# Kernel optimization log

Measured on AMD Instinct MI355X. Metric: run time of the kernel, lower is better.

## Reference

```python
import jax, jax.numpy as jnp
import numpy as np

NUM_HEADS = 16
HEAD_SIZE = 64
CTXT_LEN = 2048
N_EMBED = 1024
BATCH = 2


def setup_inputs() -> dict:
    key = jax.random.key(0)
    ks = jax.random.split(key, 5)
    s = 0.02  # realistic init scale for weights
    return {
        "x": jax.random.normal(ks[0], (BATCH, CTXT_LEN, N_EMBED), dtype=jnp.float32),
        "Wk": jax.random.normal(ks[1], (N_EMBED, NUM_HEADS * HEAD_SIZE), dtype=jnp.float32) * s,
        "bk": jnp.zeros((NUM_HEADS * HEAD_SIZE,), dtype=jnp.float32),
        "Wq": jax.random.normal(ks[2], (N_EMBED, NUM_HEADS * HEAD_SIZE), dtype=jnp.float32) * s,
        "bq": jnp.zeros((NUM_HEADS * HEAD_SIZE,), dtype=jnp.float32),
        "Wv": jax.random.normal(ks[3], (N_EMBED, NUM_HEADS * HEAD_SIZE), dtype=jnp.float32) * s,
        "bv": jnp.zeros((NUM_HEADS * HEAD_SIZE,), dtype=jnp.float32),
        "Wo": jax.random.normal(ks[4], (NUM_HEADS * HEAD_SIZE, N_EMBED), dtype=jnp.float32) * s,
        "bo": jnp.zeros((N_EMBED,), dtype=jnp.float32),
    }


def reference(x, Wk, bk, Wq, bq, Wv, bv, Wo, bo):
    B, T, E = x.shape
    H, D = NUM_HEADS, HEAD_SIZE
    # QKV projections -> [B, T, H, D]
    k = (x @ Wk + bk).reshape(B, T, H, D)
    q = (x @ Wq + bq).reshape(B, T, H, D)
    v = (x @ Wv + bv).reshape(B, T, H, D)
    # NOTE: source scales by 1/sqrt(n_embed), not 1/sqrt(head_size)
    scale = 1.0 / (E ** 0.5)
    wei = jnp.einsum('bthd,bshd->bhts', q, k) * scale  # [B, H, T, T]
    causal = jnp.tril(jnp.ones((T, T), dtype=bool))
    wei = jnp.where(causal, wei, -jnp.inf)
    wei = jax.nn.softmax(wei, axis=-1)
    # dropout p=0.0 -> identity
    out = jnp.einsum('bhts,bshd->bthd', wei, v).reshape(B, T, H * D)
    return out @ Wo + bo
```

## Files before the change

kernel.cpp:

```cpp
#include <hip/hip_runtime.h>

#define NH 16
#define HS 64
#define T_CTX 2048
#define NE 1024
#define NB 2
#define BT (NB*T_CTX)
#define HD (NH*HS)

typedef unsigned short u16;
typedef __bf16 bf16_t;
typedef bf16_t bf16x8 __attribute__((ext_vector_type(8)));
typedef float f32x4 __attribute__((ext_vector_type(4)));
typedef u16 u16x8 __attribute__((ext_vector_type(8)));
typedef u16 u16x4 __attribute__((ext_vector_type(4)));

#define GLDS(gp, lp) __builtin_amdgcn_global_load_lds( \
    (const __attribute__((address_space(1))) void*)(gp), \
    (__attribute__((address_space(3))) void*)(lp), 16, 0, 0)

__device__ __forceinline__ u16 f2bf(float f) {
  union { float f; unsigned u; } x; x.f = f;
  return (u16)((x.u + 0x7fffu + ((x.u >> 16) & 1u)) >> 16);
}
__device__ __forceinline__ float bf2f(u16 u) {
  union { unsigned u; float f; } x; x.u = ((unsigned)u) << 16;
  return x.f;
}
__device__ __forceinline__ unsigned pack_bf2(float hi, float lo) {
  union { float f; unsigned u; } H, L; H.f = hi; L.f = lo;
  return __builtin_amdgcn_perm(H.u + 0x8000u, L.u + 0x8000u, 0x07060302);
}

__global__ __launch_bounds__(256) void k_prep_x(const float* __restrict__ x,
                                                u16* __restrict__ xb) {
  int i = blockIdx.x * blockDim.x + threadIdx.x;
  float4 v = ((const float4*)x)[i];
  ushort4 o;
  o.x = f2bf(v.x); o.y = f2bf(v.y); o.z = f2bf(v.z); o.w = f2bf(v.w);
  ((ushort4*)xb)[i] = o;
}

__global__ __launch_bounds__(256) void k_prep_w(
    const float* __restrict__ W0, const float* __restrict__ W1,
    const float* __restrict__ W2, const float* __restrict__ W3,
    u16* __restrict__ T0, u16* __restrict__ T1,
    u16* __restrict__ T2, u16* __restrict__ T3) {
  const float* W; u16* T;
  switch (blockIdx.z) {
    case 0: W = W0; T = T0; break;
    case 1: W = W1; T = T1; break;
    case 2: W = W2; T = T2; break;
    default: W = W3; T = T3; break;
  }
  __shared__ u16 tile[64 * 72];
  int k0 = blockIdx.x * 64, n0 = blockIdx.y * 64;
  int tid = threadIdx.x;
#pragma unroll
  for (int it = 0; it < 4; ++it) {
    int ci = tid + it * 256;
    int k = ci >> 4, c = ci & 15;
    float4 v = *(const float4*)&W[(size_t)(k0 + k) * NE + n0 + c * 4];
    int n = c * 4;
    tile[(n + 0) * 72 + k] = f2bf(v.x);
    tile[(n + 1) * 72 + k] = f2bf(v.y);
    tile[(n + 2) * 72 + k] = f2bf(v.z);
    tile[(n + 3) * 72 + k] = f2bf(v.w);
  }
  __syncthreads();
#pragma unroll
  for (int it = 0; it < 2; ++it) {
    int co = tid + it * 256;
    int n = co >> 3, c = co & 7;
    u16x8 v = *(const u16x8*)&tile[n * 72 + c * 8];
    *(u16x8*)&T[(size_t)(n0 + n) * NE + k0 + c * 8] = v;
  }
}

__global__ __launch_bounds__(256) void k_gemm_qkv(
    const u16* __restrict__ xb, const u16* __restrict__ Wt,
    const float* __restrict__ bq, const float* __restrict__ bk,
    const float* __restrict__ bv, u16* __restrict__ Qw,
    u16* __restrict__ Kw, u16* __restrict__ Vtw) {
  __shared__ u16 sh[3 * 8192];
  const int z = blockIdx.z;
  const u16* W = Wt + (size_t)z * NE * HD;
  const float* bias = (z == 0) ? bq : (z == 1 ? bk : bv);
  const float scale = (z == 0) ? 0.03125f * 1.4426950408889634f : 1.0f;
  const int bx = blockIdx.x;
  const int xcd = bx & 7, ii = bx >> 3;
  const int m0 = (xcd + 8 * (ii & 3)) * 128;
  const int n0 = (ii >> 2) * 128;
  const int tid = threadIdx.x;
  const int lane = tid & 63, w = tid >> 6;
  const int wm = (w >> 1) * 64, wn = (w & 1) * 64, q = lane >> 4, l16 = lane & 15;
  const int qsw = q ^ ((l16 >> 1) & 3);

  auto stage = [&](int k0, int b) {
    u16* As = sh + b * 8192;
    u16* Bs = As + 4096;
#pragma unroll
    for (int s2 = 0; s2 < 2; ++s2) {
      int ci = w * 64 + lane + s2 * 256;
      int row = ci >> 2, cc = ci & 3;
      int cs = cc ^ ((row >> 1) & 3);
      GLDS(xb + (size_t)(m0 + row) * NE + k0 + cs * 8, As + (size_t)ci * 8);
      GLDS(W  + (size_t)(n0 + row) * NE + k0 + cs * 8, Bs + (size_t)ci * 8);
    }
  };

  f32x4 acc[4][4];
#pragma unroll
  for (int i = 0; i < 4; ++i)
#pragma unroll
    for (int j = 0; j < 4; ++j)
#pragma unroll
      for (int r = 0; r < 4; ++r) acc[i][j][r] = 0.f;

  stage(0, 0);
  stage(32, 1);
  for (int kt = 0; kt < 32; ++kt) {
    u16* As = sh + (kt % 3) * 8192;
    u16* Bs = As + 4096;
    if (kt + 1 < 32)
      asm volatile("s_waitcnt vmcnt(4)\n\ts_barrier" ::: "memory");
    else
      asm volatile("s_waitcnt vmcnt(0)\n\ts_barrier" ::: "memory");
    if (kt + 2 < 32) stage((kt + 2) * 32, (kt + 2) % 3);
    bf16x8 av[4], bv4[4];
#pragma unroll
    for (int i = 0; i < 4; ++i) av[i]  = *(const bf16x8*)&As[(wm + i * 16 + l16) * 32 + qsw * 8];
#pragma unroll
    for (int j = 0; j < 4; ++j) bv4[j] = *(const bf16x8*)&Bs[(wn + j * 16 + l16) * 32 + qsw * 8];
#pragma unroll
    for (int i = 0; i < 4; ++i)
#pragma unroll
      for (int j = 0; j < 4; ++j)
        acc[i][j] = __builtin_amdgcn_mfma_f32_16x16x32_bf16(av[i], bv4[j], acc[i][j], 0, 0, 0);
  }
  __syncthreads();
  u16* Es = sh;

  const int bb = m0 >> 11;
  if (z == 2) {
#pragma unroll
    for (int j = 0; j < 4; ++j) {
      int n = wn + j * 16 + l16;
      float bn = bias[n0 + n];
#pragma unroll
      for (int i = 0; i < 4; ++i) {
        int m = wm + i * 16 + q * 4;
        u16x4 pk;
#pragma unroll
        for (int r = 0; r < 4; ++r) pk[r] = f2bf(acc[i][j][r] + bn);
        *(u16x4*)&Es[n * 132 + m] = pk;
      }
    }
    __syncthreads();
#pragma unroll
    for (int it = 0; it < 8; ++it) {
      int idx = it * 256 + tid;
      int dl = idx >> 4, c = idx & 15;
      u16x8 v = *(const u16x8*)&Es[dl * 132 + c * 8];
      int ng = n0 + dl, h = ng >> 6, d = ng & 63;
      int tt = (m0 & (T_CTX - 1)) + c * 8;
      *(u16x8*)&Vtw[((size_t)((bb * NH + h) * HS + d)) * T_CTX + tt] = v;
    }
  } else {
    u16* dst = (z == 0) ? Qw : Kw;
#pragma unroll
    for (int j = 0; j < 4; ++j) {
      int n = wn + j * 16 + l16;
      float bn = bias[n0 + n];
#pragma unroll
      for (int i = 0; i < 4; ++i)
#pragma unroll
        for (int r = 0; r < 4; ++r) {
          int m = wm + i * 16 + q * 4 + r;
          Es[m * 132 + n] = f2bf((acc[i][j][r] + bn) * scale);
        }
    }
    __syncthreads();
#pragma unroll
    for (int it = 0; it < 8; ++it) {
      int idx = it * 256 + tid;
      int tl = idx >> 4, c = idx & 15;
      u16x8 v = *(const u16x8*)&Es[tl * 132 + c * 8];
      int ng = n0 + c * 8, h = ng >> 6, d = ng & 63;
      int tt = (m0 & (T_CTX - 1)) + tl;
      *(u16x8*)&dst[(((size_t)(bb * NH + h)) * T_CTX + tt) * HS + d] = v;
    }
  }
}

__device__ __forceinline__ void stage_kv(const u16* __restrict__ Kp,
                                         const u16* __restrict__ Vp,
                                         int k0, u16* KsB, u16* VsB, int tid) {
#pragma unroll
  for (int it = 0; it < 2; ++it) {
    int ci = tid + it * 256;
    int row = ci >> 3, cc = ci & 7;
    int prow = (row & 32) | ((row & 12) << 1) | ((row & 16) >> 2) | (row & 3);
    int sw = (cc ^ (row & 7)) * 8;
    GLDS(Kp + (size_t)(k0 + prow) * HS + sw, KsB + ci * 8);
    GLDS(Vp + (size_t)row * T_CTX + k0 + sw, VsB + ci * 8);
  }
}

__global__ __launch_bounds__(256) void k_attn(
    const u16* __restrict__ Qw, const u16* __restrict__ Kw,
    const u16* __restrict__ Vtw, u16* __restrict__ op0,
    u16* __restrict__ op1, u16* __restrict__ op2,
    float* __restrict__ lsum) {
  __shared__ u16 Ks[3 * 64 * 64];
  __shared__ u16 Vs[3 * 64 * 64];

  const int b = blockIdx.x;
  const int xcd = b & 7, ii = b >> 3;
  const int bh = xcd + 8 * (ii & 3);
  const int x = ii >> 2;
  const int qt = 15 - x / 3;
  const int part = x - (15 - qt) * 3;
  const int ntiles = 2 * (qt + 1);
  const int npt = (ntiles + 2) / 3;
  const int klo = part * npt;
  const int khi = min(klo + npt, ntiles);
  const int qbase = qt * 128;

  const u16* Qp = Qw + (size_t)bh * T_CTX * HS;
  const u16* Kp = Kw + (size_t)bh * T_CTX * HS;
  const u16* Vp = Vtw + (size_t)bh * HS * T_CTX;

  const int tid = threadIdx.x, lane = tid & 63, w = tid >> 6;
  const int q = lane >> 4, c = lane & 15;
  const int rbase = w * 32;

  bf16x8 aq[2][2];
#pragma unroll
  for (int i = 0; i < 2; ++i)
#pragma unroll
    for (int s = 0; s < 2; ++s)
      aq[i][s] = *(const bf16x8*)&Qp[(size_t)(qbase + rbase + i * 16 + c) * HS + s * 32 + q * 8];

  f32x4 o[2][4];
  float lrow[2] = {0.f, 0.f};
#pragma unroll
  for (int i = 0; i < 2; ++i)
#pragma unroll
    for (int j = 0; j < 4; ++j)
#pragma unroll
      for (int r = 0; r < 4; ++r) o[i][j][r] = 0.f;

  if (klo < khi)     stage_kv(Kp, Vp, klo * 64,       Ks,        Vs,        tid);
  if (klo + 1 < khi) stage_kv(Kp, Vp, (klo + 1) * 64, Ks + 4096, Vs + 4096, tid);

  for (int kt = klo; kt < khi; ++kt) {
    const int k0 = kt * 64;
    const int idx = kt - klo;
    u16* KsB = Ks + (idx % 3) * 4096;
    u16* VsB = Vs + (idx % 3) * 4096;
    if (kt + 1 < khi) {
      asm volatile("s_waitcnt vmcnt(4)\n\ts_barrier" ::: "memory");
    } else {
      asm volatile("s_waitcnt vmcnt(0)\n\ts_barrier" ::: "memory");
    }
    if (kt + 2 < khi)
      stage_kv(Kp, Vp, (kt + 2) * 64,
               Ks + ((idx + 2) % 3) * 4096, Vs + ((idx + 2) % 3) * 4096, tid);

    f32x4 s[4][2];
#pragma unroll
    for (int i2 = 0; i2 < 4; ++i2) {
      int krow = i2 * 16 + c;
      bf16x8 kf0 = *(const bf16x8*)&KsB[krow * 64 + ((0 + q) ^ (krow & 7)) * 8];
      bf16x8 kf1 = *(const bf16x8*)&KsB[krow * 64 + ((4 + q) ^ (krow & 7)) * 8];
#pragma unroll
      for (int j2 = 0; j2 < 2; ++j2) {
        f32x4 z4 = {0.f, 0.f, 0.f, 0.f};
        z4 = __builtin_amdgcn_mfma_f32_16x16x32_bf16(kf0, aq[j2][0], z4, 0, 0, 0);
        s[i2][j2] = __builtin_amdgcn_mfma_f32_16x16x32_bf16(kf1, aq[j2][1], z4, 0, 0, 0);
      }
    }

    if (k0 + 63 > qbase + rbase) {
#pragma unroll
      for (int i2 = 0; i2 < 4; ++i2)
#pragma unroll
        for (int j2 = 0; j2 < 2; ++j2)
#pragma unroll
          for (int r = 0; r < 4; ++r) {
            int key = k0 + ((i2 >> 1) << 5) + (q << 3) + ((i2 & 1) << 2) + r;
            int qrow = qbase + rbase + j2 * 16 + c;
            if (key > qrow) s[i2][j2][r] = -1e30f;
          }
    }

#pragma unroll
    for (int i2 = 0; i2 < 4; ++i2)
#pragma unroll
      for (int j2 = 0; j2 < 2; ++j2)
#pragma unroll
        for (int r = 0; r < 4; ++r) {
          float p = __builtin_amdgcn_exp2f(s[i2][j2][r]);
          s[i2][j2][r] = p;
          lrow[j2] += p;
        }

#pragma unroll
    for (int ks = 0; ks < 2; ++ks) {
      bf16x8 bv4[4];
#pragma unroll
      for (int j = 0; j < 4; ++j) {
        int d = j * 16 + c;
        bv4[j] = *(const bf16x8*)&VsB[d * 64 + ((ks * 4 + q) ^ (d & 7)) * 8];
      }
#pragma unroll
      for (int i = 0; i < 2; ++i) {
        union { uint4 u; bf16x8 b; } af;
        af.u.x = pack_bf2(s[2 * ks][i][1],     s[2 * ks][i][0]);
        af.u.y = pack_bf2(s[2 * ks][i][3],     s[2 * ks][i][2]);
        af.u.z = pack_bf2(s[2 * ks + 1][i][1], s[2 * ks + 1][i][0]);
        af.u.w = pack_bf2(s[2 * ks + 1][i][3], s[2 * ks + 1][i][2]);
#pragma unroll
        for (int j = 0; j < 4; ++j)
          o[i][j] = __builtin_amdgcn_mfma_f32_16x16x32_bf16(af.b, bv4[j], o[i][j], 0, 0, 0);
      }
    }
  }

  u16* op = (part == 0) ? op0 : (part == 1 ? op1 : op2);
  const size_t row0 = (size_t)bh * T_CTX + qbase;
#pragma unroll
  for (int i = 0; i < 2; ++i) {
    lrow[i] += __shfl_xor(lrow[i], 16, 64);
    lrow[i] += __shfl_xor(lrow[i], 32, 64);
  }
  if (q == 0) {
#pragma unroll
    for (int i = 0; i < 2; ++i)
      lsum[(size_t)part * 65536 + row0 + rbase + i * 16 + c] = lrow[i];
  }
#pragma unroll
  for (int i = 0; i < 2; ++i)
#pragma unroll
    for (int r = 0; r < 4; ++r) {
      size_t t = row0 + rbase + i * 16 + q * 4 + r;
#pragma unroll
      for (int j = 0; j < 4; ++j)
        op[t * 64 + j * 16 + c] = f2bf(o[i][j][r]);
    }
}

__global__ __launch_bounds__(256) void k_combine(
    const u16* __restrict__ op0, const u16* __restrict__ op1,
    const u16* __restrict__ op2, const float* __restrict__ lsum,
    u16* __restrict__ att) {
  int idx = blockIdx.x * 256 + threadIdx.x;
  int row = idx >> 3, oct = idx & 7;
  float l0 = lsum[row], l1 = lsum[65536 + row], l2 = lsum[131072 + row];
  float inv = 1.f / (l0 + l1 + l2);
  u16x8 a = *(const u16x8*)&op0[(size_t)row * 64 + oct * 8];
  u16x8 b = *(const u16x8*)&op1[(size_t)row * 64 + oct * 8];
  u16x8 d = *(const u16x8*)&op2[(size_t)row * 64 + oct * 8];
  u16x8 ov;
#pragma unroll
  for (int e = 0; e < 8; ++e)
    ov[e] = f2bf((bf2f(a[e]) + bf2f(b[e]) + bf2f(d[e])) * inv);
  int bh = row >> 11, t = row & 2047, bb = bh >> 4, h = bh & 15;
  *(u16x8*)&att[((size_t)(bb * T_CTX + t)) * HD + h * 64 + oct * 8] = ov;
}

__global__ __launch_bounds__(256) void k_gemm_out(
    const u16* __restrict__ attb, const u16* __restrict__ Wot,
    const float* __restrict__ bo, float* __restrict__ out) {
  __shared__ u16 sh[3 * 6144];
  const int bx = blockIdx.x;
  const int xcd = bx & 7, ii = bx >> 3;
  const int m0 = (xcd + 8 * (ii & 7)) * 64;
  const int n0 = (ii >> 3) * 128;
  const int tid = threadIdx.x, lane = tid & 63, w = tid >> 6;
  const int wm = (w & 1) * 32, wn = (w >> 1) * 64;
  const int q = lane >> 4, l16 = lane & 15;
  const int qsw = q ^ ((l16 >> 1) & 3);

  auto stage = [&](int k0, int b) {
    u16* As = sh + b * 6144;
    u16* Bs = As + 2048;
    {
      int row = tid >> 2, cc = tid & 3;
      int cs = cc ^ ((row >> 1) & 3);
      GLDS(attb + (size_t)(m0 + row) * NE + k0 + cs * 8, As + (size_t)tid * 8);
    }
#pragma unroll
    for (int s2 = 0; s2 < 2; ++s2) {
      int ci = tid + s2 * 256;
      int row = ci >> 2, cc = ci & 3;
      int cs = cc ^ ((row >> 1) & 3);
      GLDS(Wot + (size_t)(n0 + row) * NE + k0 + cs * 8, Bs + (size_t)ci * 8);
    }
  };

  f32x4 acc[2][4];
#pragma unroll
  for (int i = 0; i < 2; ++i)
#pragma unroll
    for (int j = 0; j < 4; ++j)
#pragma unroll
      for (int r = 0; r < 4; ++r) acc[i][j][r] = 0.f;

  stage(0, 0);
  stage(32, 1);
  for (int kt = 0; kt < 32; ++kt) {
    u16* As = sh + (kt % 3) * 6144;
    u16* Bs = As + 2048;
    if (kt + 1 < 32)
      asm volatile("s_waitcnt vmcnt(3)\n\ts_barrier" ::: "memory");
    else
      asm volatile("s_waitcnt vmcnt(0)\n\ts_barrier" ::: "memory");
    if (kt + 2 < 32) stage((kt + 2) * 32, (kt + 2) % 3);
    bf16x8 av[2], bv4[4];
#pragma unroll
    for (int i = 0; i < 2; ++i) av[i]  = *(const bf16x8*)&As[(wm + i * 16 + l16) * 32 + qsw * 8];
#pragma unroll
    for (int j = 0; j < 4; ++j) bv4[j] = *(const bf16x8*)&Bs[(wn + j * 16 + l16) * 32 + qsw * 8];
#pragma unroll
    for (int i = 0; i < 2; ++i)
#pragma unroll
      for (int j = 0; j < 4; ++j)
        acc[i][j] = __builtin_amdgcn_mfma_f32_16x16x32_bf16(av[i], bv4[j], acc[i][j], 0, 0, 0);
  }
#pragma unroll
  for (int j = 0; j < 4; ++j) {
    int n = n0 + wn + j * 16 + l16;
    float bn = bo[n];
#pragma unroll
    for (int i = 0; i < 2; ++i)
#pragma unroll
      for (int r = 0; r < 4; ++r) {
        int m = m0 + wm + i * 16 + q * 4 + r;
        out[(size_t)m * NE + n] = acc[i][j][r] + bn;
      }
  }
}

extern "C" void kernel_launch(void* const* d_in, const int* in_sizes, int n_in,
                              void* d_out, int out_size, void* d_ws, size_t ws_size,
                              hipStream_t stream) {
  (void)in_sizes; (void)n_in; (void)out_size; (void)ws_size;
  const float* x  = (const float*)d_in[0];
  const float* Wk = (const float*)d_in[1];
  const float* bk = (const float*)d_in[2];
  const float* Wq = (const float*)d_in[3];
  const float* bq = (const float*)d_in[4];
  const float* Wv = (const float*)d_in[5];
  const float* bv = (const float*)d_in[6];
  const float* Wo = (const float*)d_in[7];
  const float* bo = (const float*)d_in[8];
  float* out = (float*)d_out;

  u16* base = (u16*)d_ws;
  const size_t M = 1024 * 1024;
  u16* xb   = base;
  u16* Wt   = base + 4 * M;
  u16* Wot  = base + 7 * M;
  u16* Qw   = base + 8 * M;
  u16* Kw   = base + 12 * M;
  u16* Vtw  = base + 16 * M;
  u16* op0  = base + 20 * M;
  u16* op1  = base + 24 * M;
  u16* op2  = base;
  float* lsum = (float*)(base + 4 * M);
  u16* attw = base + 12 * M;

  k_prep_x<<<dim3(BT * NE / 4 / 256), 256, 0, stream>>>(x, xb);
  k_prep_w<<<dim3(16, 16, 4), 256, 0, stream>>>(
      Wq, Wk, Wv, Wo, Wt, Wt + (size_t)NE * HD, Wt + (size_t)2 * NE * HD, Wot);
  k_gemm_qkv<<<dim3(256, 1, 3), 256, 0, stream>>>(xb, Wt, bq, bk, bv, Qw, Kw, Vtw);
  k_attn<<<dim3(1536), 256, 0, stream>>>(Qw, Kw, Vtw, op0, op1, op2, lsum);
  k_combine<<<dim3(2048), 256, 0, stream>>>(op0, op1, op2, lsum, attw);
  k_gemm_out<<<dim3(512), 256, 0, stream>>>(attw, Wot, bo, out);
}
```

Measured before the change: 186.1 us.

## Restructure QKV GEMM into 256x256 tiles with 8 waves and interleaved staging

Rewrites the fused QKV projection GEMM to use 256x256 output tiles computed by 512-thread blocks (8 waves, each 128x64), with a BK=64 double-buffered LDS pipeline and an XOR swizzle. Global-to-LDS loads for the next k-tile are split into four chunks and issued between MFMA groups, and s_setprio raises wave priority around the MFMA bursts. The three Q/K/V projections are folded into a single 192-block grid, and the epilogue writes through LDS in two row-halves. The aim is more operand reuse per byte loaded and better overlap of loads with MFMA work. In exchange it uses 128 KB of LDS per block and far more accumulator registers per thread, and it launches fewer, larger blocks, which may leave some CUs underused.

```diff
diff --git a/kernel.cpp b/kernel.cpp
--- a/kernel.cpp
+++ b/kernel.cpp
@@ -77,118 +77,198 @@
   }
 }
 
-__global__ __launch_bounds__(256) void k_gemm_qkv(
+__global__ __launch_bounds__(512, 2) void k_gemm_qkv(
     const u16* __restrict__ xb, const u16* __restrict__ Wt,
     const float* __restrict__ bq, const float* __restrict__ bk,
     const float* __restrict__ bv, u16* __restrict__ Qw,
     u16* __restrict__ Kw, u16* __restrict__ Vtw) {
-  __shared__ u16 sh[3 * 8192];
-  const int z = blockIdx.z;
-  const u16* W = Wt + (size_t)z * NE * HD;
-  const float* bias = (z == 0) ? bq : (z == 1 ? bk : bv);
-  const float scale = (z == 0) ? 0.03125f * 1.4426950408889634f : 1.0f;
-  const int bx = blockIdx.x;
-  const int xcd = bx & 7, ii = bx >> 3;
-  const int m0 = (xcd + 8 * (ii & 3)) * 128;
-  const int n0 = (ii >> 2) * 128;
-  const int tid = threadIdx.x;
-  const int lane = tid & 63, w = tid >> 6;
-  const int wm = (w >> 1) * 64, wn = (w & 1) * 64, q = lane >> 4, l16 = lane & 15;
-  const int qsw = q ^ ((l16 >> 1) & 3);
-
-  auto stage = [&](int k0, int b) {
-    u16* As = sh + b * 8192;
-    u16* Bs = As + 4096;
+  __shared__ u16 sh[65536];
+  const int b = blockIdx.x;
+  const int xcd = b & 7, ii = b >> 3;
+  const int mt = xcd * 2 + (ii & 1);
+  const int nt = ii >> 1;
+  const int m0g = mt * 256;
+  const size_t n0g = (size_t)nt * 256;
+
+  const int tid = threadIdx.x, lane = tid & 63, w = tid >> 6;
+  const int wr = w >> 2, wc = w & 3;
+  const int l16 = lane & 15, q = lane >> 4;
+
+  auto stageA = [&](int tt, int h) {
+    u16* dst = sh + (h * 2 + (tt & 1)) * 8192;
+    const u16* src = xb + (size_t)(m0g + h * 128) * NE + tt * 64;
 #pragma unroll
     for (int s2 = 0; s2 < 2; ++s2) {
-      int ci = w * 64 + lane + s2 * 256;
-      int row = ci >> 2, cc = ci & 3;
-      int cs = cc ^ ((row >> 1) & 3);
-      GLDS(xb + (size_t)(m0 + row) * NE + k0 + cs * 8, As + (size_t)ci * 8);
-      GLDS(W  + (size_t)(n0 + row) * NE + k0 + cs * 8, Bs + (size_t)ci * 8);
+      int ci = tid + s2 * 512;
+      int row = ci >> 3, c = ci & 7;
+      int cs = c ^ (row & 7);
+      GLDS(src + (size_t)row * NE + cs * 8, dst + ci * 8);
     }
   };
-
-  f32x4 acc[4][4];
-#pragma unroll
-  for (int i = 0; i < 4; ++i)
+  auto stageB = [&](int tt, int h) {
+    u16* dst = sh + 32768 + (h * 2 + (tt & 1)) * 8192;
+    const u16* src = Wt + (n0g + h * 128) * NE + tt * 64;
+#pragma unroll
+    for (int s2 = 0; s2 < 2; ++s2) {
+      int ci = tid + s2 * 512;
+      int row = ci >> 3, c = ci & 7;
+      int cs = c ^ (row & 7);
+      GLDS(src + (size_t)row * NE + cs * 8, dst + ci * 8);
+    }
+  };
+  auto ldA = [&](int p, int i, int s) {
+    int r = i * 16 + l16;
+    return *(const bf16x8*)&sh[(wr * 2 + p) * 8192 + r * 64 +
+                               ((s * 4 + q) ^ (r & 7)) * 8];
+  };
+  auto ldB = [&](int p, int j, int s) {
+    int r = (wc & 1) * 64 + j * 16 + l16;
+    return *(const bf16x8*)&sh[32768 + ((wc >> 1) * 2 + p) * 8192 + r * 64 +
+                               ((s * 4 + q) ^ (r & 7)) * 8];
+  };
+
+  f32x4 acc[8][4];
+#pragma unroll
+  for (int i = 0; i < 8; ++i)
 #pragma unroll
     for (int j = 0; j < 4; ++j)
 #pragma unroll
       for (int r = 0; r < 4; ++r) acc[i][j][r] = 0.f;
 
-  stage(0, 0);
-  stage(32, 1);
-  for (int kt = 0; kt < 32; ++kt) {
-    u16* As = sh + (kt % 3) * 8192;
-    u16* Bs = As + 4096;
-    if (kt + 1 < 32)
-      asm volatile("s_waitcnt vmcnt(4)\n\ts_barrier" ::: "memory");
+  stageA(0, 0); stageA(0, 1); stageB(0, 0); stageB(0, 1);
+  stageA(1, 0); stageA(1, 1); stageB(1, 0); stageB(1, 1);
+  asm volatile("s_waitcnt vmcnt(8)\n\ts_barrier" ::: "memory");
+
+  bf16x8 a[4][2], bfr[4][2];
+#pragma unroll 1
+  for (int t = 0; t < 16; ++t) {
+    const int p = t & 1;
+#pragma unroll
+    for (int i = 0; i < 4; ++i) { a[i][0] = ldA(p, i, 0); a[i][1] = ldA(p, i, 1); }
+#pragma unroll
+    for (int j = 0; j < 4; ++j) { bfr[j][0] = ldB(p, j, 0); bfr[j][1] = ldB(p, j, 1); }
+    asm volatile("s_barrier" ::: "memory");
+    __builtin_amdgcn_s_setprio(1);
+#pragma unroll
+    for (int s = 0; s < 2; ++s)
+#pragma unroll
+      for (int i = 0; i < 4; ++i)
+#pragma unroll
+        for (int j = 0; j < 2; ++j)
+          acc[i][j] = __builtin_amdgcn_mfma_f32_16x16x32_bf16(a[i][s], bfr[j][s], acc[i][j], 0, 0, 0);
+    __builtin_amdgcn_s_setprio(0);
+    asm volatile("s_barrier" ::: "memory");
+    if (t + 2 < 16) stageB(t + 2, 0);
+    asm volatile("s_barrier" ::: "memory");
+    __builtin_amdgcn_s_setprio(1);
+#pragma unroll
+    for (int s = 0; s < 2; ++s)
+#pragma unroll
+      for (int i = 0; i < 4; ++i)
+#pragma unroll
+        for (int j = 0; j < 2; ++j)
+          acc[i][j + 2] = __builtin_amdgcn_mfma_f32_16x16x32_bf16(a[i][s], bfr[j + 2][s], acc[i][j + 2], 0, 0, 0);
+    __builtin_amdgcn_s_setprio(0);
+    asm volatile("s_barrier" ::: "memory");
+#pragma unroll
+    for (int i = 0; i < 4; ++i) { a[i][0] = ldA(p, i + 4, 0); a[i][1] = ldA(p, i + 4, 1); }
+    if (t + 2 < 16) stageB(t + 2, 1);
+    asm volatile("s_barrier" ::: "memory");
+    __builtin_amdgcn_s_setprio(1);
+#pragma unroll
+    for (int s = 0; s < 2; ++s)
+#pragma unroll
+      for (int i = 0; i < 4; ++i)
+#pragma unroll
+        for (int j = 0; j < 2; ++j)
+          acc[i + 4][j] = __builtin_amdgcn_mfma_f32_16x16x32_bf16(a[i][s], bfr[j][s], acc[i + 4][j], 0, 0, 0);
+    __builtin_amdgcn_s_setprio(0);
+    asm volatile("s_barrier" ::: "memory");
+    if (t + 2 < 16) { stageA(t + 2, 0); stageA(t + 2, 1); }
+    asm volatile("s_barrier" ::: "memory");
+    __builtin_amdgcn_s_setprio(1);
+#pragma unroll
+    for (int s = 0; s < 2; ++s)
+#pragma unroll
+      for (int i = 0; i < 4; ++i)
+#pragma unroll
+        for (int j = 0; j < 2; ++j)
+          acc[i + 4][j + 2] = __builtin_amdgcn_mfma_f32_16x16x32_bf16(a[i][s], bfr[j + 2][s], acc[i + 4][j + 2], 0, 0, 0);
+    __builtin_amdgcn_s_setprio(0);
+    if (t + 2 < 16)
+      asm volatile("s_waitcnt vmcnt(8)\n\ts_barrier" ::: "memory");
+    else if (t + 1 < 16)
+      asm volatile("s_waitcnt vmcnt(0)\n\ts_barrier" ::: "memory");
     else
-      asm volatile("s_waitcnt vmcnt(0)\n\ts_barrier" ::: "memory");
-    if (kt + 2 < 32) stage((kt + 2) * 32, (kt + 2) % 3);
-    bf16x8 av[4], bv4[4];
-#pragma unroll
-    for (int i = 0; i < 4; ++i) av[i]  = *(const bf16x8*)&As[(wm + i * 16 + l16) * 32 + qsw * 8];
-#pragma unroll
-    for (int j = 0; j < 4; ++j) bv4[j] = *(const bf16x8*)&Bs[(wn + j * 16 + l16) * 32 + qsw * 8];
-#pragma unroll
-    for (int i = 0; i < 4; ++i)
-#pragma unroll
-      for (int j = 0; j < 4; ++j)
-        acc[i][j] = __builtin_amdgcn_mfma_f32_16x16x32_bf16(av[i], bv4[j], acc[i][j], 0, 0, 0);
-  }
-  __syncthreads();
+      asm volatile("s_barrier" ::: "memory");
+  }
+
   u16* Es = sh;
-
-  const int bb = m0 >> 11;
-  if (z == 2) {
-#pragma unroll
-    for (int j = 0; j < 4; ++j) {
-      int n = wn + j * 16 + l16;
-      float bn = bias[n0 + n];
-#pragma unroll
-      for (int i = 0; i < 4; ++i) {
-        int m = wm + i * 16 + q * 4;
-        u16x4 pk;
-#pragma unroll
-        for (int r = 0; r < 4; ++r) pk[r] = f2bf(acc[i][j][r] + bn);
-        *(u16x4*)&Es[n * 132 + m] = pk;
-      }
-    }
-    __syncthreads();
-#pragma unroll
-    for (int it = 0; it < 8; ++it) {
-      int idx = it * 256 + tid;
-      int dl = idx >> 4, c = idx & 15;
-      u16x8 v = *(const u16x8*)&Es[dl * 132 + c * 8];
-      int ng = n0 + dl, h = ng >> 6, d = ng & 63;
-      int tt = (m0 & (T_CTX - 1)) + c * 8;
-      *(u16x8*)&Vtw[((size_t)((bb * NH + h) * HS + d)) * T_CTX + tt] = v;
+  const int z = nt >> 2;
+  const int n0z = (nt & 3) * 256;
+  const int bb = m0g >> 11;
+  if (z <= 1) {
+    const float* bias = (z == 0) ? bq : bk;
+    const float scale = (z == 0) ? 0.03125f * 1.4426950408889634f : 1.0f;
+    u16* dst = (z == 0) ? Qw : Kw;
+#pragma unroll 1
+    for (int ph = 0; ph < 2; ++ph) {
+      __syncthreads();
+      if (wr == ph) {
+#pragma unroll
+        for (int j = 0; j < 4; ++j) {
+          int n = wc * 64 + j * 16 + l16;
+          float bn = bias[n0z + n];
+#pragma unroll
+          for (int i = 0; i < 8; ++i)
+#pragma unroll
+            for (int r = 0; r < 4; ++r) {
+              int m = i * 16 + q * 4 + r;
+              Es[m * 264 + n] = f2bf((acc[i][j][r] + bn) * scale);
+            }
+        }
+      }
+      __syncthreads();
+#pragma unroll
+      for (int it = 0; it < 8; ++it) {
+        int idx = it * 512 + tid;
+        int tl = idx >> 5, c = idx & 31;
+        u16x8 v = *(const u16x8*)&Es[tl * 264 + c * 8];
+        int ng = n0z + c * 8, h = ng >> 6, d = ng & 63;
+        int mg = m0g + ph * 128 + tl;
+        int tt2 = mg & (T_CTX - 1);
+        *(u16x8*)&dst[(((size_t)(bb * NH + h)) * T_CTX + tt2) * HS + d] = v;
+      }
     }
   } else {
-    u16* dst = (z == 0) ? Qw : Kw;
-#pragma unroll
-    for (int j = 0; j < 4; ++j) {
-      int n = wn + j * 16 + l16;
-      float bn = bias[n0 + n];
-#pragma unroll
-      for (int i = 0; i < 4; ++i)
-#pragma unroll
-        for (int r = 0; r < 4; ++r) {
-          int m = wm + i * 16 + q * 4 + r;
-          Es[m * 132 + n] = f2bf((acc[i][j][r] + bn) * scale);
+#pragma unroll 1
+    for (int ph = 0; ph < 2; ++ph) {
+      __syncthreads();
+      if (wr == ph) {
+#pragma unroll
+        for (int j = 0; j < 4; ++j) {
+          int n = wc * 64 + j * 16 + l16;
+          float bn = bv[n0z + n];
+#pragma unroll
+          for (int i = 0; i < 8; ++i) {
+            int m = i * 16 + q * 4;
+            u16x4 pk;
+#pragma unroll
+            for (int r = 0; r < 4; ++r) pk[r] = f2bf(acc[i][j][r] + bn);
+            *(u16x4*)&Es[n * 136 + m] = pk;
+          }
         }
-    }
-    __syncthreads();
-#pragma unroll
-    for (int it = 0; it < 8; ++it) {
-      int idx = it * 256 + tid;
-      int tl = idx >> 4, c = idx & 15;
-      u16x8 v = *(const u16x8*)&Es[tl * 132 + c * 8];
-      int ng = n0 + c * 8, h = ng >> 6, d = ng & 63;
-      int tt = (m0 & (T_CTX - 1)) + tl;
-      *(u16x8*)&dst[(((size_t)(bb * NH + h)) * T_CTX + tt) * HS + d] = v;
+      }
+      __syncthreads();
+#pragma unroll
+      for (int it = 0; it < 8; ++it) {
+        int idx = it * 512 + tid;
+        int dl = idx >> 4, c = idx & 15;
+        u16x8 v = *(const u16x8*)&Es[dl * 136 + c * 8];
+        int ng = n0z + dl, h = ng >> 6, d = ng & 63;
+        int tt2 = (m0g & (T_CTX - 1)) + ph * 128 + c * 8;
+        *(u16x8*)&Vtw[(((size_t)(bb * NH + h)) * HS + d) * T_CTX + tt2] = v;
+      }
     }
   }
 }
@@ -475,7 +555,7 @@
   k_prep_x<<<dim3(BT * NE / 4 / 256), 256, 0, stream>>>(x, xb);
   k_prep_w<<<dim3(16, 16, 4), 256, 0, stream>>>(
       Wq, Wk, Wv, Wo, Wt, Wt + (size_t)NE * HD, Wt + (size_t)2 * NE * HD, Wot);
-  k_gemm_qkv<<<dim3(256, 1, 3), 256, 0, stream>>>(xb, Wt, bq, bk, bv, Qw, Kw, Vtw);
+  k_gemm_qkv<<<dim3(192), 512, 0, stream>>>(xb, Wt, bq, bk, bv, Qw, Kw, Vtw);
   k_attn<<<dim3(1536), 256, 0, stream>>>(Qw, Kw, Vtw, op0, op1, op2, lsum);
   k_combine<<<dim3(2048), 256, 0, stream>>>(op0, op1, op2, lsum, attw);
   k_gemm_out<<<dim3(512), 256, 0, stream>>>(attw, Wot, bo, out);
```

Measured after the change: 184.6 us. About the same (-0.8%).
